# Kernel optimization log

Hardware: AMD Instinct MI355X
Metric: run time of the kernel (lower is better)

The kernel has to match this reference:

```python
import jax, jax.numpy as jnp
import numpy as np

WH, WW = 16, 16          # window size
S = WH * WW              # tokens per window = 256
B = 128                  # batch of windows
E = 1024                 # embed_dim
H = 16                   # num_heads
D = E // H               # head_dim = 64


def _swin_rel_index():
    # Swin-style relative position index, identical to the torch buffer construction
    coords = np.stack(np.meshgrid(np.arange(WH), np.arange(WW), indexing='ij'))  # [2,WH,WW]
    cf = coords.reshape(2, -1)                         # [2, S]
    rel = cf[:, :, None] - cf[:, None, :]              # [2, S, S]
    rel = rel.transpose(1, 2, 0).copy()                # [S, S, 2]
    rel[..., 0] += WH - 1
    rel[..., 1] += WW - 1
    rel[..., 0] *= 2 * WW - 1
    return rel.sum(-1).astype(np.int32)                # [S, S] in [0, (2WH-1)(2WW-1))


def setup_inputs() -> dict:
    key = jax.random.key(0)
    ks = jax.random.split(key, 6)
    x = jax.random.normal(ks[0], (B, S, E), dtype=jnp.float32)
    qkv_w = jax.random.normal(ks[1], (3 * E, E), dtype=jnp.float32) * 0.02
    qkv_b = jax.random.normal(ks[2], (3 * E,), dtype=jnp.float32) * 0.02
    out_w = jax.random.normal(ks[3], (E, E), dtype=jnp.float32) * 0.02
    out_b = jax.random.normal(ks[4], (E,), dtype=jnp.float32) * 0.02
    bias_table = jax.random.normal(ks[5], ((2 * WH - 1) * (2 * WW - 1), H), dtype=jnp.float32) * 0.02
    rel_index = jnp.asarray(_swin_rel_index())
    return {"x": x, "qkv_w": qkv_w, "qkv_b": qkv_b, "out_w": out_w,
            "out_b": out_b, "bias_table": bias_table, "rel_index": rel_index,
            "x_ignored_": 0, "x_ignored_1_": 0}


def reference(x, qkv_w, qkv_b, out_w, out_b, bias_table, rel_index, x_ignored_, x_ignored_1_):
    b, s, e = x.shape
    h = bias_table.shape[-1]
    d = e // h
    # fused QKV projection
    qkv = x @ qkv_w.T + qkv_b                          # [b, s, 3e]
    qkv = qkv.reshape(b, s, 3, h, d)
    q, k, v = qkv[:, :, 0], qkv[:, :, 1], qkv[:, :, 2]  # [b, s, h, d]
    scale = d ** -0.5
    # learned relative position bias, [h, s, s]
    bias = bias_table[rel_index.reshape(-1)].reshape(s, s, h).transpose(2, 0, 1)
    scores = jnp.einsum('bqhd,bkhd->bhqk', q, k) * scale + bias[None]
    attn = jax.nn.softmax(scores, axis=-1)
    ctx = jnp.einsum('bhqk,bkhd->bqhd', attn, v).reshape(b, s, e)
    return ctx @ out_w.T + out_b
```

## Files before the change

kernel.cpp:

```cpp
#include <hip/hip_runtime.h>
#include <stdint.h>

#define BB 128
#define SS 256
#define EE 1024
#define HH 16
#define DD 64
#define MM (BB*SS)

typedef __attribute__((ext_vector_type(8))) short bf16x8;
typedef __attribute__((ext_vector_type(4))) float f32x4;

__device__ __forceinline__ unsigned short f2bf(float f) {
  union { float f; unsigned int u; } c; c.f = f;
  unsigned int u = c.u;
  u += 0x7fffu + ((u >> 16) & 1u);
  return (unsigned short)(u >> 16);
}

__device__ __forceinline__ void gld16(const unsigned short* g, unsigned short* l) {
  __builtin_amdgcn_global_load_lds((__attribute__((address_space(1))) void*)(g),
                                   (__attribute__((address_space(3))) void*)(l), 16, 0, 0);
}

__global__ __launch_bounds__(256) void cast_x_kernel(const float4* __restrict__ x,
                                                     ushort4* __restrict__ o, int n4) {
  int stride = gridDim.x * blockDim.x;
  for (int i = blockIdx.x * blockDim.x + threadIdx.x; i < n4; i += stride) {
    float4 v = x[i];
    ushort4 r;
    r.x = f2bf(v.x); r.y = f2bf(v.y); r.z = f2bf(v.z); r.w = f2bf(v.w);
    o[i] = r;
  }
}

__global__ __launch_bounds__(256) void prep_kernel(const float4* __restrict__ qw,
                                                   const float4* __restrict__ ow,
                                                   const float* __restrict__ btab,
                                                   const int* __restrict__ ridx,
                                                   ushort4* __restrict__ qwb,
                                                   ushort4* __restrict__ owb,
                                                   float* __restrict__ biasmat) {
  const int NQ = (3 * EE * EE) / 4;
  const int NO = (EE * EE) / 4;
  const int NBIAS = HH * SS * SS;
  const int total = NQ + NO + NBIAS;
  int stride = gridDim.x * blockDim.x;
  for (int i = blockIdx.x * blockDim.x + threadIdx.x; i < total; i += stride) {
    if (i < NQ) {
      float4 v = qw[i];
      ushort4 r; r.x = f2bf(v.x); r.y = f2bf(v.y); r.z = f2bf(v.z); r.w = f2bf(v.w);
      qwb[i] = r;
    } else if (i < NQ + NO) {
      int t = i - NQ;
      float4 v = ow[t];
      ushort4 r; r.x = f2bf(v.x); r.y = f2bf(v.y); r.z = f2bf(v.z); r.w = f2bf(v.w);
      owb[t] = r;
    } else {
      int t = i - (NQ + NO);
      int h = t >> 16;
      int ij = t & 65535;
      biasmat[t] = btab[ridx[ij] * HH + h];
    }
  }
}

__device__ __forceinline__ void gemm_mainloop(const unsigned short* __restrict__ A,
                                              const unsigned short* __restrict__ Bw,
                                              unsigned short* As, unsigned short* Bs,
                                              int row0, int col0, int K,
                                              f32x4 acc[4][4]) {
  const int tid = threadIdx.x;
  const int wave = tid >> 6, lane = tid & 63;
  const int wm = wave & 1, wn = wave >> 1;
  const int l15 = lane & 15, quad = lane >> 4;
  const int ldrow = lane >> 2, ldc = lane & 3;
  const unsigned short* agp0 = A + (size_t)(row0 + wave * 16 + ldrow) * K + ldc * 8;
  const unsigned short* agp1 = A + (size_t)(row0 + (4 + wave) * 16 + ldrow) * K + ldc * 8;
  const unsigned short* bgp0 = Bw + (size_t)(col0 + wave * 16 + ldrow) * K + ldc * 8;
  const unsigned short* bgp1 = Bw + (size_t)(col0 + (4 + wave) * 16 + ldrow) * K + ldc * 8;
  unsigned short* al0 = As + wave * 512;
  unsigned short* al1 = As + (4 + wave) * 512;
  unsigned short* bl0 = Bs + wave * 512;
  unsigned short* bl1 = Bs + (4 + wave) * 512;
  for (int k0 = 0; k0 < K; k0 += 32) {
    gld16(agp0 + k0, al0);
    gld16(agp1 + k0, al1);
    gld16(bgp0 + k0, bl0);
    gld16(bgp1 + k0, bl1);
    __syncthreads();
    bf16x8 af[4], bfm[4];
#pragma unroll
    for (int i = 0; i < 4; ++i)
      af[i] = *(const bf16x8*)(As + (wm * 64 + i * 16 + l15) * 32 + quad * 8);
#pragma unroll
    for (int j = 0; j < 4; ++j)
      bfm[j] = *(const bf16x8*)(Bs + (wn * 64 + j * 16 + l15) * 32 + quad * 8);
#pragma unroll
    for (int i = 0; i < 4; ++i)
#pragma unroll
      for (int j = 0; j < 4; ++j)
        acc[i][j] = __builtin_amdgcn_mfma_f32_16x16x32_bf16(af[i], bfm[j], acc[i][j], 0, 0, 0);
    __syncthreads();
  }
}

__global__ __launch_bounds__(256) void qkv_gemm(const unsigned short* __restrict__ A,
                                                const unsigned short* __restrict__ Bw,
                                                const float* __restrict__ bias,
                                                unsigned short* __restrict__ q,
                                                unsigned short* __restrict__ kx,
                                                unsigned short* __restrict__ vt) {
  __shared__ unsigned short As[128 * 32];
  __shared__ unsigned short Bs[128 * 32];
  const int tid = threadIdx.x;
  const int wave = tid >> 6, lane = tid & 63;
  const int wm = wave & 1, wn = wave >> 1;
  const int l15 = lane & 15, quad = lane >> 4;
  const int row0 = blockIdx.x * 128;
  const int col0 = blockIdx.y * 128;
  f32x4 acc[4][4];
#pragma unroll
  for (int i = 0; i < 4; ++i)
#pragma unroll
    for (int j = 0; j < 4; ++j) acc[i][j] = (f32x4){0.f, 0.f, 0.f, 0.f};
  gemm_mainloop(A, Bw, As, Bs, row0, col0, EE, acc);
  const int which = col0 >> 10;
#pragma unroll
  for (int i = 0; i < 4; ++i) {
    const int mbase = row0 + wm * 64 + i * 16 + quad * 4;
    const int bb = mbase >> 8;
    const int s0 = mbase & 255;
#pragma unroll
    for (int j = 0; j < 4; ++j) {
      const int n = col0 + wn * 64 + j * 16 + l15;
      const int hn = (n >> 6) & 15;
      const int d = n & 63;
      const float bv = bias[n];
      if (which == 0) {
        size_t base = ((size_t)(bb * HH + hn) * SS + s0) * DD + d;
#pragma unroll
        for (int r = 0; r < 4; ++r)
          q[base + (size_t)r * DD] = f2bf((acc[i][j][r] + bv) * 0.125f);
      } else if (which == 1) {
        size_t base = ((size_t)(bb * HH + hn) * SS + s0) * DD + d;
#pragma unroll
        for (int r = 0; r < 4; ++r)
          kx[base + (size_t)r * DD] = f2bf(acc[i][j][r] + bv);
      } else {
        size_t base = ((size_t)(bb * HH + hn) * DD + d) * SS + s0;
        ushort4 pk;
        pk.x = f2bf(acc[i][j][0] + bv);
        pk.y = f2bf(acc[i][j][1] + bv);
        pk.z = f2bf(acc[i][j][2] + bv);
        pk.w = f2bf(acc[i][j][3] + bv);
        *(ushort4*)(vt + base) = pk;
      }
    }
  }
}

__global__ __launch_bounds__(256) void attn_kernel(const unsigned short* __restrict__ q,
                                                   const unsigned short* __restrict__ kx,
                                                   const unsigned short* __restrict__ vt,
                                                   const float* __restrict__ biasmat,
                                                   unsigned short* __restrict__ ctx) {
  __shared__ unsigned short P[4][16 * 264];
  const int tid = threadIdx.x;
  const int wave = tid >> 6, lane = tid & 63;
  const int l15 = lane & 15, quad = lane >> 4;
  const int qblk = blockIdx.x & 3;
  const int bh = blockIdx.x >> 2;
  const int h = bh & 15;
  const int b_ = bh >> 4;
  const unsigned short* qp = q + (size_t)bh * SS * DD;
  const unsigned short* kp = kx + (size_t)bh * SS * DD;
  const unsigned short* vp = vt + (size_t)bh * SS * DD;
  const float* bp = biasmat + (size_t)h * SS * SS;
  const int qr0 = qblk * 64 + wave * 16;

  bf16x8 aq0 = *(const bf16x8*)(qp + (qr0 + l15) * DD + quad * 8);
  bf16x8 aq1 = *(const bf16x8*)(qp + (qr0 + l15) * DD + 32 + quad * 8);

  f32x4 sacc[16];
#pragma unroll
  for (int j = 0; j < 16; ++j) sacc[j] = (f32x4){0.f, 0.f, 0.f, 0.f};
#pragma unroll
  for (int j = 0; j < 16; ++j) {
    bf16x8 b0 = *(const bf16x8*)(kp + (j * 16 + l15) * DD + quad * 8);
    bf16x8 b1 = *(const bf16x8*)(kp + (j * 16 + l15) * DD + 32 + quad * 8);
    sacc[j] = __builtin_amdgcn_mfma_f32_16x16x32_bf16(aq0, b0, sacc[j], 0, 0, 0);
    sacc[j] = __builtin_amdgcn_mfma_f32_16x16x32_bf16(aq1, b1, sacc[j], 0, 0, 0);
  }
  const int rbase = qr0 + quad * 4;
  float mx[4] = {-1e30f, -1e30f, -1e30f, -1e30f};
#pragma unroll
  for (int j = 0; j < 16; ++j)
#pragma unroll
    for (int r = 0; r < 4; ++r) {
      float v = sacc[j][r] + bp[(rbase + r) * SS + j * 16 + l15];
      sacc[j][r] = v;
      mx[r] = fmaxf(mx[r], v);
    }
#pragma unroll
  for (int r = 0; r < 4; ++r)
#pragma unroll
    for (int m = 8; m >= 1; m >>= 1) mx[r] = fmaxf(mx[r], __shfl_xor(mx[r], m, 16));
  float sum[4] = {0.f, 0.f, 0.f, 0.f};
#pragma unroll
  for (int j = 0; j < 16; ++j)
#pragma unroll
    for (int r = 0; r < 4; ++r) {
      float e = __expf(sacc[j][r] - mx[r]);
      sacc[j][r] = e;
      sum[r] += e;
    }
#pragma unroll
  for (int r = 0; r < 4; ++r) {
#pragma unroll
    for (int m = 8; m >= 1; m >>= 1) sum[r] += __shfl_xor(sum[r], m, 16);
    sum[r] = 1.f / sum[r];
  }
  unsigned short* Pw = &P[wave][0];
#pragma unroll
  for (int j = 0; j < 16; ++j)
#pragma unroll
    for (int r = 0; r < 4; ++r)
      Pw[(quad * 4 + r) * 264 + j * 16 + l15] = f2bf(sacc[j][r] * sum[r]);
  __syncthreads();
  f32x4 cacc[4];
#pragma unroll
  for (int nt = 0; nt < 4; ++nt) cacc[nt] = (f32x4){0.f, 0.f, 0.f, 0.f};
#pragma unroll
  for (int kk = 0; kk < 8; ++kk) {
    bf16x8 a = *(const bf16x8*)(Pw + l15 * 264 + kk * 32 + quad * 8);
#pragma unroll
    for (int nt = 0; nt < 4; ++nt) {
      bf16x8 b = *(const bf16x8*)(vp + (nt * 16 + l15) * SS + kk * 32 + quad * 8);
      cacc[nt] = __builtin_amdgcn_mfma_f32_16x16x32_bf16(a, b, cacc[nt], 0, 0, 0);
    }
  }
#pragma unroll
  for (int nt = 0; nt < 4; ++nt)
#pragma unroll
    for (int r = 0; r < 4; ++r)
      ctx[(size_t)(b_ * SS + qr0 + quad * 4 + r) * EE + h * DD + nt * 16 + l15] =
          f2bf(cacc[nt][r]);
}

__global__ __launch_bounds__(256) void out_gemm(const unsigned short* __restrict__ A,
                                                const unsigned short* __restrict__ Bw,
                                                const float* __restrict__ bias,
                                                float* __restrict__ out) {
  __shared__ unsigned short As[128 * 32];
  __shared__ unsigned short Bs[128 * 32];
  const int tid = threadIdx.x;
  const int wave = tid >> 6, lane = tid & 63;
  const int wm = wave & 1, wn = wave >> 1;
  const int l15 = lane & 15, quad = lane >> 4;
  const int row0 = blockIdx.x * 128;
  const int col0 = blockIdx.y * 128;
  f32x4 acc[4][4];
#pragma unroll
  for (int i = 0; i < 4; ++i)
#pragma unroll
    for (int j = 0; j < 4; ++j) acc[i][j] = (f32x4){0.f, 0.f, 0.f, 0.f};
  gemm_mainloop(A, Bw, As, Bs, row0, col0, EE, acc);
#pragma unroll
  for (int i = 0; i < 4; ++i) {
    const int m0 = row0 + wm * 64 + i * 16 + quad * 4;
#pragma unroll
    for (int j = 0; j < 4; ++j) {
      const int n = col0 + wn * 64 + j * 16 + l15;
      const float bv = bias[n];
#pragma unroll
      for (int r = 0; r < 4; ++r)
        out[(size_t)(m0 + r) * EE + n] = acc[i][j][r] + bv;
    }
  }
}

#define WS_XCTX  ((size_t)0)
#define WS_QKVW  ((size_t)67108864)
#define WS_OUTW  ((size_t)73400320)
#define WS_BIAS  ((size_t)75497472)
#define WS_Q     ((size_t)79691776)
#define WS_K     ((size_t)146800640)
#define WS_VT    ((size_t)213909504)

extern "C" void kernel_launch(void* const* d_in, const int* in_sizes, int n_in,
                              void* d_out, int out_size, void* d_ws, size_t ws_size,
                              hipStream_t stream) {
  (void)in_sizes; (void)n_in; (void)out_size; (void)ws_size;
  const float* x      = (const float*)d_in[0];
  const float* qkv_w  = (const float*)d_in[1];
  const float* qkv_b  = (const float*)d_in[2];
  const float* out_w  = (const float*)d_in[3];
  const float* out_b  = (const float*)d_in[4];
  const float* btab   = (const float*)d_in[5];
  const int*   ridx   = (const int*)d_in[6];
  float* out = (float*)d_out;
  char* ws = (char*)d_ws;

  unsigned short* xctx  = (unsigned short*)(ws + WS_XCTX);
  unsigned short* qkvwb = (unsigned short*)(ws + WS_QKVW);
  unsigned short* outwb = (unsigned short*)(ws + WS_OUTW);
  float*          biasm = (float*)(ws + WS_BIAS);
  unsigned short* q     = (unsigned short*)(ws + WS_Q);
  unsigned short* k     = (unsigned short*)(ws + WS_K);
  unsigned short* vt    = (unsigned short*)(ws + WS_VT);

  cast_x_kernel<<<4096, 256, 0, stream>>>((const float4*)x, (ushort4*)xctx,
                                          (MM * EE) / 4);
  prep_kernel<<<2048, 256, 0, stream>>>((const float4*)qkv_w, (const float4*)out_w,
                                        btab, ridx,
                                        (ushort4*)qkvwb, (ushort4*)outwb, biasm);
  qkv_gemm<<<dim3(MM / 128, (3 * EE) / 128), 256, 0, stream>>>(xctx, qkvwb, qkv_b,
                                                               q, k, vt);
  attn_kernel<<<BB * HH * (SS / 64), 256, 0, stream>>>(q, k, vt, biasm, xctx);
  out_gemm<<<dim3(MM / 128, EE / 128), 256, 0, stream>>>(xctx, outwb, out_b, out);
}
```

Measured before the change: 854.1 us.

## Fuse casts, swizzle GEMM LDS, restructure attention with LDS K and exp2 softmax

```diff
diff --git a/kernel.cpp b/kernel.cpp
--- a/kernel.cpp
+++ b/kernel.cpp
@@ -8,6 +8,8 @@
 #define DD 64
 #define MM (BB*SS)
 
+#define LOG2E 1.44269504088896f
+
 typedef __attribute__((ext_vector_type(8))) short bf16x8;
 typedef __attribute__((ext_vector_type(4))) float f32x4;
 
@@ -18,49 +20,65 @@
   return (unsigned short)(u >> 16);
 }
 
+__device__ __forceinline__ float fast_exp2(float x) {
+#if __has_builtin(__builtin_amdgcn_exp2f)
+  return __builtin_amdgcn_exp2f(x);
+#else
+  return exp2f(x);
+#endif
+}
+
+__device__ __forceinline__ float fast_rcp(float x) {
+#if __has_builtin(__builtin_amdgcn_rcpf)
+  return __builtin_amdgcn_rcpf(x);
+#else
+  return 1.0f / x;
+#endif
+}
+
 __device__ __forceinline__ void gld16(const unsigned short* g, unsigned short* l) {
   __builtin_amdgcn_global_load_lds((__attribute__((address_space(1))) void*)(g),
                                    (__attribute__((address_space(3))) void*)(l), 16, 0, 0);
 }
 
-__global__ __launch_bounds__(256) void cast_x_kernel(const float4* __restrict__ x,
-                                                     ushort4* __restrict__ o, int n4) {
-  int stride = gridDim.x * blockDim.x;
-  for (int i = blockIdx.x * blockDim.x + threadIdx.x; i < n4; i += stride) {
-    float4 v = x[i];
-    ushort4 r;
-    r.x = f2bf(v.x); r.y = f2bf(v.y); r.z = f2bf(v.z); r.w = f2bf(v.w);
-    o[i] = r;
-  }
-}
-
-__global__ __launch_bounds__(256) void prep_kernel(const float4* __restrict__ qw,
+__global__ __launch_bounds__(256) void prep_kernel(const float4* __restrict__ x4,
+                                                   const float4* __restrict__ qw,
                                                    const float4* __restrict__ ow,
                                                    const float* __restrict__ btab,
                                                    const int* __restrict__ ridx,
+                                                   ushort4* __restrict__ xb,
                                                    ushort4* __restrict__ qwb,
                                                    ushort4* __restrict__ owb,
-                                                   float* __restrict__ biasmat) {
+                                                   float* __restrict__ biasC) {
+  const int NX = (MM * EE) / 4;
   const int NQ = (3 * EE * EE) / 4;
   const int NO = (EE * EE) / 4;
   const int NBIAS = HH * SS * SS;
-  const int total = NQ + NO + NBIAS;
+  const int total = NX + NQ + NO + NBIAS;
   int stride = gridDim.x * blockDim.x;
   for (int i = blockIdx.x * blockDim.x + threadIdx.x; i < total; i += stride) {
-    if (i < NQ) {
-      float4 v = qw[i];
+    if (i < NX) {
+      float4 v = x4[i];
       ushort4 r; r.x = f2bf(v.x); r.y = f2bf(v.y); r.z = f2bf(v.z); r.w = f2bf(v.w);
-      qwb[i] = r;
-    } else if (i < NQ + NO) {
-      int t = i - NQ;
+      xb[i] = r;
+    } else if (i < NX + NQ) {
+      int t = i - NX;
+      float4 v = qw[t];
+      ushort4 r; r.x = f2bf(v.x); r.y = f2bf(v.y); r.z = f2bf(v.z); r.w = f2bf(v.w);
+      qwb[t] = r;
+    } else if (i < NX + NQ + NO) {
+      int t = i - (NX + NQ);
       float4 v = ow[t];
       ushort4 r; r.x = f2bf(v.x); r.y = f2bf(v.y); r.z = f2bf(v.z); r.w = f2bf(v.w);
       owb[t] = r;
     } else {
-      int t = i - (NQ + NO);
-      int h = t >> 16;
-      int ij = t & 65535;
-      biasmat[t] = btab[ridx[ij] * HH + h];
+      int t = i - (NX + NQ + NO);
+      int h   = t >> 16;
+      int row = (t >> 8) & 255;
+      int lo  = (t >> 4) & 15;
+      int hi  = t & 15;
+      int col = hi * 16 + lo;
+      biasC[t] = btab[ridx[row * SS + col] * HH + h] * LOG2E;
     }
   }
 }
@@ -75,10 +93,12 @@
   const int wm = wave & 1, wn = wave >> 1;
   const int l15 = lane & 15, quad = lane >> 4;
   const int ldrow = lane >> 2, ldc = lane & 3;
-  const unsigned short* agp0 = A + (size_t)(row0 + wave * 16 + ldrow) * K + ldc * 8;
-  const unsigned short* agp1 = A + (size_t)(row0 + (4 + wave) * 16 + ldrow) * K + ldc * 8;
-  const unsigned short* bgp0 = Bw + (size_t)(col0 + wave * 16 + ldrow) * K + ldc * 8;
-  const unsigned short* bgp1 = Bw + (size_t)(col0 + (4 + wave) * 16 + ldrow) * K + ldc * 8;
+  const int gsw = (ldc ^ ((ldrow >> 1) & 3)) * 8;
+  const int rsw = (l15 >> 1) & 3;
+  const unsigned short* agp0 = A + (size_t)(row0 + wave * 16 + ldrow) * K + gsw;
+  const unsigned short* agp1 = A + (size_t)(row0 + (4 + wave) * 16 + ldrow) * K + gsw;
+  const unsigned short* bgp0 = Bw + (size_t)(col0 + wave * 16 + ldrow) * K + gsw;
+  const unsigned short* bgp1 = Bw + (size_t)(col0 + (4 + wave) * 16 + ldrow) * K + gsw;
   unsigned short* al0 = As + wave * 512;
   unsigned short* al1 = As + (4 + wave) * 512;
   unsigned short* bl0 = Bs + wave * 512;
@@ -92,10 +112,10 @@
     bf16x8 af[4], bfm[4];
 #pragma unroll
     for (int i = 0; i < 4; ++i)
-      af[i] = *(const bf16x8*)(As + (wm * 64 + i * 16 + l15) * 32 + quad * 8);
+      af[i] = *(const bf16x8*)(As + (wm * 64 + i * 16 + l15) * 32 + (quad ^ rsw) * 8);
 #pragma unroll
     for (int j = 0; j < 4; ++j)
-      bfm[j] = *(const bf16x8*)(Bs + (wn * 64 + j * 16 + l15) * 32 + quad * 8);
+      bfm[j] = *(const bf16x8*)(Bs + (wn * 64 + j * 16 + l15) * 32 + (quad ^ rsw) * 8);
 #pragma unroll
     for (int i = 0; i < 4; ++i)
 #pragma unroll
@@ -126,6 +146,7 @@
     for (int j = 0; j < 4; ++j) acc[i][j] = (f32x4){0.f, 0.f, 0.f, 0.f};
   gemm_mainloop(A, Bw, As, Bs, row0, col0, EE, acc);
   const int which = col0 >> 10;
+  const float QS = 0.125f * LOG2E;
 #pragma unroll
   for (int i = 0; i < 4; ++i) {
     const int mbase = row0 + wm * 64 + i * 16 + quad * 4;
@@ -141,7 +162,7 @@
         size_t base = ((size_t)(bb * HH + hn) * SS + s0) * DD + d;
 #pragma unroll
         for (int r = 0; r < 4; ++r)
-          q[base + (size_t)r * DD] = f2bf((acc[i][j][r] + bv) * 0.125f);
+          q[base + (size_t)r * DD] = f2bf((acc[i][j][r] + bv) * QS);
       } else if (which == 1) {
         size_t base = ((size_t)(bb * HH + hn) * SS + s0) * DD + d;
 #pragma unroll
@@ -163,89 +184,94 @@
 __global__ __launch_bounds__(256) void attn_kernel(const unsigned short* __restrict__ q,
                                                    const unsigned short* __restrict__ kx,
                                                    const unsigned short* __restrict__ vt,
-                                                   const float* __restrict__ biasmat,
+                                                   const float* __restrict__ biasC,
                                                    unsigned short* __restrict__ ctx) {
-  __shared__ unsigned short P[4][16 * 264];
+  __shared__ unsigned short Ks[256 * 64];
+  __shared__ unsigned short P[4][16 * 256];
   const int tid = threadIdx.x;
   const int wave = tid >> 6, lane = tid & 63;
   const int l15 = lane & 15, quad = lane >> 4;
-  const int qblk = blockIdx.x & 3;
-  const int bh = blockIdx.x >> 2;
+  const int swl = l15 & 7;
+  const int bh = blockIdx.x;
   const int h = bh & 15;
   const int b_ = bh >> 4;
   const unsigned short* qp = q + (size_t)bh * SS * DD;
   const unsigned short* kp = kx + (size_t)bh * SS * DD;
   const unsigned short* vp = vt + (size_t)bh * SS * DD;
-  const float* bp = biasmat + (size_t)h * SS * SS;
-  const int qr0 = qblk * 64 + wave * 16;
-
-  bf16x8 aq0 = *(const bf16x8*)(qp + (qr0 + l15) * DD + quad * 8);
-  bf16x8 aq1 = *(const bf16x8*)(qp + (qr0 + l15) * DD + 32 + quad * 8);
-
-  f32x4 sacc[16];
-#pragma unroll
-  for (int j = 0; j < 16; ++j) sacc[j] = (f32x4){0.f, 0.f, 0.f, 0.f};
-#pragma unroll
-  for (int j = 0; j < 16; ++j) {
-    bf16x8 b0 = *(const bf16x8*)(kp + (j * 16 + l15) * DD + quad * 8);
-    bf16x8 b1 = *(const bf16x8*)(kp + (j * 16 + l15) * DD + 32 + quad * 8);
-    sacc[j] = __builtin_amdgcn_mfma_f32_16x16x32_bf16(aq0, b0, sacc[j], 0, 0, 0);
-    sacc[j] = __builtin_amdgcn_mfma_f32_16x16x32_bf16(aq1, b1, sacc[j], 0, 0, 0);
-  }
-  const int rbase = qr0 + quad * 4;
-  float mx[4] = {-1e30f, -1e30f, -1e30f, -1e30f};
-#pragma unroll
-  for (int j = 0; j < 16; ++j)
+
+#pragma unroll
+  for (int rr = 0; rr < 8; ++rr) {
+    int gc = rr * 256 + tid;
+    int row = gc >> 3, sc = gc & 7;
+    int c = sc ^ (row & 7);
+    gld16(kp + row * 64 + c * 8, Ks + (rr * 256 + wave * 64) * 8);
+  }
+  __syncthreads();
+
+  unsigned short* Pw = &P[wave][0];
+  for (int qblk = 0; qblk < 4; ++qblk) {
+    const int qr0 = qblk * 64 + wave * 16;
+    bf16x8 aq0 = *(const bf16x8*)(qp + (qr0 + l15) * DD + quad * 8);
+    bf16x8 aq1 = *(const bf16x8*)(qp + (qr0 + l15) * DD + 32 + quad * 8);
+
+    f32x4 sacc[16];
+#pragma unroll
+    for (int j = 0; j < 16; ++j) sacc[j] = (f32x4){0.f, 0.f, 0.f, 0.f};
+#pragma unroll
+    for (int j = 0; j < 16; ++j) {
+      const unsigned short* krow = Ks + (j * 16 + l15) * 64;
+      bf16x8 b0 = *(const bf16x8*)(krow + (quad ^ swl) * 8);
+      bf16x8 b1 = *(const bf16x8*)(krow + ((4 + quad) ^ swl) * 8);
+      sacc[j] = __builtin_amdgcn_mfma_f32_16x16x32_bf16(aq0, b0, sacc[j], 0, 0, 0);
+      sacc[j] = __builtin_amdgcn_mfma_f32_16x16x32_bf16(aq1, b1, sacc[j], 0, 0, 0);
+    }
 #pragma unroll
     for (int r = 0; r < 4; ++r) {
-      float v = sacc[j][r] + bp[(rbase + r) * SS + j * 16 + l15];
-      sacc[j][r] = v;
-      mx[r] = fmaxf(mx[r], v);
-    }
-#pragma unroll
-  for (int r = 0; r < 4; ++r)
-#pragma unroll
-    for (int m = 8; m >= 1; m >>= 1) mx[r] = fmaxf(mx[r], __shfl_xor(mx[r], m, 16));
-  float sum[4] = {0.f, 0.f, 0.f, 0.f};
-#pragma unroll
-  for (int j = 0; j < 16; ++j)
-#pragma unroll
-    for (int r = 0; r < 4; ++r) {
-      float e = __expf(sacc[j][r] - mx[r]);
-      sacc[j][r] = e;
-      sum[r] += e;
-    }
-#pragma unroll
-  for (int r = 0; r < 4; ++r) {
-#pragma unroll
-    for (int m = 8; m >= 1; m >>= 1) sum[r] += __shfl_xor(sum[r], m, 16);
-    sum[r] = 1.f / sum[r];
-  }
-  unsigned short* Pw = &P[wave][0];
-#pragma unroll
-  for (int j = 0; j < 16; ++j)
-#pragma unroll
-    for (int r = 0; r < 4; ++r)
-      Pw[(quad * 4 + r) * 264 + j * 16 + l15] = f2bf(sacc[j][r] * sum[r]);
-  __syncthreads();
-  f32x4 cacc[4];
-#pragma unroll
-  for (int nt = 0; nt < 4; ++nt) cacc[nt] = (f32x4){0.f, 0.f, 0.f, 0.f};
-#pragma unroll
-  for (int kk = 0; kk < 8; ++kk) {
-    bf16x8 a = *(const bf16x8*)(Pw + l15 * 264 + kk * 32 + quad * 8);
-#pragma unroll
-    for (int nt = 0; nt < 4; ++nt) {
-      bf16x8 b = *(const bf16x8*)(vp + (nt * 16 + l15) * SS + kk * 32 + quad * 8);
-      cacc[nt] = __builtin_amdgcn_mfma_f32_16x16x32_bf16(a, b, cacc[nt], 0, 0, 0);
-    }
-  }
-#pragma unroll
-  for (int nt = 0; nt < 4; ++nt)
-#pragma unroll
-    for (int r = 0; r < 4; ++r)
-      ctx[(size_t)(b_ * SS + qr0 + quad * 4 + r) * EE + h * DD + nt * 16 + l15] =
-          f2bf(cacc[nt][r]);
+      const int prow = quad * 4 + r;
+      const float* bC = biasC + ((size_t)((h * 256 + qr0 + prow) * 16 + l15)) * 16;
+      float4 bv0 = ((const float4*)bC)[0];
+      float4 bv1 = ((const float4*)bC)[1];
+      float4 bv2 = ((const float4*)bC)[2];
+      float4 bv3 = ((const float4*)bC)[3];
+      float bj[16] = {bv0.x, bv0.y, bv0.z, bv0.w, bv1.x, bv1.y, bv1.z, bv1.w,
+                      bv2.x, bv2.y, bv2.z, bv2.w, bv3.x, bv3.y, bv3.z, bv3.w};
+      float s = 0.f;
+#pragma unroll
+      for (int j = 0; j < 16; ++j) {
+        float e = fast_exp2(sacc[j][r] + bj[j]);
+        sacc[j][r] = e;
+        s += e;
+      }
+#pragma unroll
+      for (int m = 8; m >= 1; m >>= 1) s += __shfl_xor(s, m, 16);
+      float rs = fast_rcp(s);
+      const int psw = prow & 7;
+#pragma unroll
+      for (int j = 0; j < 16; ++j) {
+        union { float f; unsigned int u; } cv; cv.f = sacc[j][r] * rs;
+        unsigned short pb = (unsigned short)((cv.u + 0x8000u) >> 16);
+        Pw[prow * 256 + (((2 * j + (l15 >> 3)) ^ psw) << 3) + swl] = pb;
+      }
+    }
+    f32x4 cacc[4];
+#pragma unroll
+    for (int nt = 0; nt < 4; ++nt) cacc[nt] = (f32x4){0.f, 0.f, 0.f, 0.f};
+#pragma unroll
+    for (int kk = 0; kk < 8; ++kk) {
+      bf16x8 a = *(const bf16x8*)(Pw + l15 * 256 + (((kk * 4 + quad) ^ swl) << 3));
+#pragma unroll
+      for (int nt = 0; nt < 4; ++nt) {
+        bf16x8 b = *(const bf16x8*)(vp + (nt * 16 + l15) * SS + kk * 32 + quad * 8);
+        cacc[nt] = __builtin_amdgcn_mfma_f32_16x16x32_bf16(a, b, cacc[nt], 0, 0, 0);
+      }
+    }
+#pragma unroll
+    for (int nt = 0; nt < 4; ++nt)
+#pragma unroll
+      for (int r = 0; r < 4; ++r)
+        ctx[(size_t)(b_ * SS + qr0 + quad * 4 + r) * EE + h * DD + nt * 16 + l15] =
+            f2bf(cacc[nt][r]);
+  }
 }
 
 __global__ __launch_bounds__(256) void out_gemm(const unsigned short* __restrict__ A,
@@ -305,18 +331,17 @@
   unsigned short* xctx  = (unsigned short*)(ws + WS_XCTX);
   unsigned short* qkvwb = (unsigned short*)(ws + WS_QKVW);
   unsigned short* outwb = (unsigned short*)(ws + WS_OUTW);
-  float*          biasm = (float*)(ws + WS_BIAS);
+  float*          biasC = (float*)(ws + WS_BIAS);
   unsigned short* q     = (unsigned short*)(ws + WS_Q);
   unsigned short* k     = (unsigned short*)(ws + WS_K);
   unsigned short* vt    = (unsigned short*)(ws + WS_VT);
 
-  cast_x_kernel<<<4096, 256, 0, stream>>>((const float4*)x, (ushort4*)xctx,
-                                          (MM * EE) / 4);
-  prep_kernel<<<2048, 256, 0, stream>>>((const float4*)qkv_w, (const float4*)out_w,
-                                        btab, ridx,
-                                        (ushort4*)qkvwb, (ushort4*)outwb, biasm);
+  prep_kernel<<<8192, 256, 0, stream>>>((const float4*)x, (const float4*)qkv_w,
+                                        (const float4*)out_w, btab, ridx,
+                                        (ushort4*)xctx, (ushort4*)qkvwb,
+                                        (ushort4*)outwb, biasC);
   qkv_gemm<<<dim3(MM / 128, (3 * EE) / 128), 256, 0, stream>>>(xctx, qkvwb, qkv_b,
                                                                q, k, vt);
-  attn_kernel<<<BB * HH * (SS / 64), 256, 0, stream>>>(q, k, vt, biasm, xctx);
+  attn_kernel<<<BB * HH, 256, 0, stream>>>(q, k, vt, biasC, xctx);
   out_gemm<<<dim3(MM / 128, EE / 128), 256, 0, stream>>>(xctx, outwb, out_b, out);
 }
```

Measured after the change: 786.8 us. 7.9% less time.
